# Kernel tuning notes

Measured on AMD Instinct MI355X. Metric: run time of the kernel, lower is better.

## Reference

```python
import jax, jax.numpy as jnp
import numpy as np

GAMMA = 1.1
PC_MIN_XY, PC_MAX_XY = -75.2, 75.2


def setup_inputs() -> dict:
    key = jax.random.key(0)
    k1, k2, k3, k4, k5 = jax.random.split(key, 5)
    N, B, F = 200000, 256, 5
    # points: x,y in pc range, z in [-2,4], remaining features small
    xy = jax.random.uniform(k1, (N, 2), minval=PC_MIN_XY, maxval=PC_MAX_XY)
    z = jax.random.uniform(k2, (N, 1), minval=-2.0, maxval=4.0)
    feat = jax.random.normal(k3, (N, F - 3)) * 0.1
    cur_points = jnp.concatenate([xy, z, feat], axis=-1).astype(jnp.float32)
    # boxes: cx,cy,cz, dx,dy (sizes ~1..6 m), dz, heading
    centers = jax.random.uniform(k4, (B, 3), minval=PC_MIN_XY, maxval=PC_MAX_XY)
    sizes = jax.random.uniform(k5, (B, 3), minval=1.0, maxval=6.0)
    heading = jnp.zeros((B, 1), dtype=jnp.float32)
    cur_boxes = jnp.concatenate([centers, sizes, heading], axis=-1).astype(jnp.float32)
    return {"cur_points": cur_points, "cur_boxes": cur_boxes, "num_sample": 128}


def reference(cur_points, cur_boxes, num_sample):
    # cylindrical_pool: radius-mask + topk + gather (N >= num_sample, so no pad)
    # radii of cylinders: ||(dx,dy)/2|| * gamma  -> [B]
    cur_radiis = jnp.linalg.norm(cur_boxes[:, 3:5] * 0.5, axis=-1) * GAMMA
    # pairwise xy distance [B, N]
    dis = jnp.linalg.norm(cur_points[None, :, :2] - cur_boxes[:, None, :2], axis=-1)
    point_mask = (dis <= cur_radiis[:, None]).astype(cur_points.dtype)  # [B, N]
    # topk over 0/1 mask: in-radius points first (ties -> lowest index, like torch)
    sampled_mask, sampled_idx = jax.lax.top_k(point_mask, num_sample)  # [B, S]
    sampled_points = cur_points[sampled_idx]  # [B, S, F] gather
    sampled_points = jnp.where(sampled_mask[..., None] > 0, sampled_points, 0.0)
    return sampled_points
```

## Files before the change

kernel.cpp:

```cpp
#include <hip/hip_runtime.h>

#define GAMMA_F 1.1f
#define F_DIM 5
#define BOXG 8
#define MAX_NSEG 256
#define MAXL 1024

__device__ __forceinline__ int prefix_lt(unsigned long long m) {
  return __builtin_amdgcn_mbcnt_hi(
      (unsigned)(m >> 32), __builtin_amdgcn_mbcnt_lo((unsigned)m, 0u));
}

template <int NWAVE>
__global__ void __launch_bounds__(NWAVE * 64, 8) seg_lds_kernel(
    const float* __restrict__ pts, const float* __restrict__ boxes,
    int* __restrict__ cnt, unsigned short* __restrict__ idx, int N, int S,
    int NSEG, int L, int NGRP) {
  __shared__ __align__(16) float2 sxy[MAXL];

  const int tid = threadIdx.x;
  const int lane = tid & 63;
  const int wid = tid >> 6;
  const int bpg = NGRP / NWAVE;
  const int seg = blockIdx.x / bpg;
  const int bg = blockIdx.x - seg * bpg;
  const int grp = bg * NWAVE + wid;
  const int box0 = grp * BOXG;

  const int start = seg * L;
  const int end = min(start + L, N);
  const int npts = end - start;

  float cx[BOXG], cy[BOXG], smax[BOXG];
#pragma unroll
  for (int b = 0; b < BOXG; ++b) {
    const float* bx = boxes + (box0 + b) * 7;
    cx[b] = bx[0];
    cy[b] = bx[1];
    const float hdx = __fmul_rn(bx[3], 0.5f);
    const float hdy = __fmul_rn(bx[4], 0.5f);
    const float r = __fmul_rn(
        __fsqrt_rn(__fadd_rn(__fmul_rn(hdx, hdx), __fmul_rn(hdy, hdy))),
        GAMMA_F);
    const unsigned ru = __float_as_uint(r);
    const float rsucc = __uint_as_float(ru + 1u);
    const double m = ((double)r + (double)rsucc) * 0.5;
    const double m2 = m * m;
    const bool incl = ((ru & 1u) == 0u);
    const float c1 = (float)m2;
    const double c1d = (double)c1;
    const bool keep = incl ? (c1d <= m2) : (c1d < m2);
    smax[b] = keep ? c1 : __uint_as_float(__float_as_uint(c1) - 1u);
  }

  for (int t = tid; t < npts; t += NWAVE * 64) {
    const float* p = pts + (size_t)(start + t) * F_DIM;
    sxy[t] = make_float2(p[0], p[1]);
  }
  __syncthreads();

  int c[BOXG];
#pragma unroll
  for (int b = 0; b < BOXG; ++b) c[b] = 0;

  const size_t ibase = ((size_t)box0 * NSEG + seg) * S;
  const float4* sxy4 = (const float4*)sxy;

#define PROCESS_8(RELBASE, X0, Y0, X1, Y1, G0, G1)                          \
  {                                                                         \
    const int rel = (RELBASE) + 2 * lane;                                   \
    _Pragma("unroll") for (int b = 0; b < BOXG; ++b) {                      \
      const float dx0 = __fsub_rn((X0), cx[b]);                             \
      const float dy0 = __fsub_rn((Y0), cy[b]);                             \
      const float s0 = __fadd_rn(__fmul_rn(dx0, dx0), __fmul_rn(dy0, dy0)); \
      const float dx1 = __fsub_rn((X1), cx[b]);                             \
      const float dy1 = __fsub_rn((Y1), cy[b]);                             \
      const float s1 = __fadd_rn(__fmul_rn(dx1, dx1), __fmul_rn(dy1, dy1)); \
      const bool sel0 = (G0) && (s0 <= smax[b]);                            \
      const bool sel1 = (G1) && (s1 <= smax[b]);                            \
      const unsigned long long m0 = __ballot(sel0);                         \
      const unsigned long long m1 = __ballot(sel1);                         \
      if (m0 | m1) {                                                        \
        const int p0 = prefix_lt(m0);                                       \
        const int p1 = prefix_lt(m1);                                       \
        const int r0 = c[b] + p0 + p1;                                      \
        const int r1 = c[b] + p0 + (sel0 ? 1 : 0) + p1;                     \
        unsigned short* mp = idx + ibase + (size_t)b * NSEG * S;            \
        if (sel0 && r0 < S) mp[r0] = (unsigned short)rel;                   \
        if (sel1 && r1 < S) mp[r1] = (unsigned short)(rel + 1);             \
        c[b] += __popcll(m0) + __popcll(m1);                                \
      }                                                                     \
    }                                                                       \
  }

  const int nfull = npts / 128;
  for (int it = 0; it < nfull; ++it) {
    const float4 q = sxy4[it * 64 + lane];
    PROCESS_8(it * 128, q.x, q.y, q.z, q.w, true, true);
  }
  const int relb = nfull * 128;
  if (relb < npts) {
    const float4 q = sxy4[nfull * 64 + lane];
    const int rel = relb + 2 * lane;
    const bool g0 = (rel < npts);
    const bool g1 = (rel + 1 < npts);
    PROCESS_8(relb, q.x, q.y, q.z, q.w, g0, g1);
  }
#undef PROCESS_8

  if (lane == 0) {
#pragma unroll
    for (int b = 0; b < BOXG; ++b) cnt[(box0 + b) * NSEG + seg] = min(c[b], S);
  }
}

__global__ void __launch_bounds__(256) gather_kernel(
    const float* __restrict__ pts, const int* __restrict__ cnt,
    const unsigned short* __restrict__ idx, float* __restrict__ out, int N,
    int S, int NSEG, int L) {
  const int b = blockIdx.x;
  const int tid = threadIdx.x;
  const int lane = tid & 63;
  const int wid = tid >> 6;

  __shared__ int pfx[MAX_NSEG + 1];
  __shared__ int wtot[4];
  __shared__ int woff[4];

  int v = (tid < NSEG) ? cnt[b * NSEG + tid] : 0;
  int sv = v;
#pragma unroll
  for (int d = 1; d < 64; d <<= 1) {
    const int t = __shfl_up(sv, d, 64);
    if (lane >= d) sv += t;
  }
  if (lane == 63) wtot[wid] = sv;
  __syncthreads();
  if (tid == 0) {
    int a = 0;
#pragma unroll
    for (int w = 0; w < 4; ++w) {
      woff[w] = a;
      a += wtot[w];
    }
  }
  __syncthreads();
  const int incl = sv + woff[wid];
  if (tid < NSEG) pfx[tid + 1] = incl;
  if (tid == 0) pfx[0] = 0;
  __syncthreads();

  const int total = pfx[NSEG];
  if (tid < S) {
    float* o = out + ((size_t)b * S + tid) * F_DIM;
    if (tid < total) {
      int lo = 0, hi = NSEG - 1;
      while (lo < hi) {
        const int mid = (lo + hi + 1) >> 1;
        if (pfx[mid] <= tid) lo = mid;
        else hi = mid - 1;
      }
      const int s = lo;
      const int gi =
          s * L + (int)idx[((size_t)b * NSEG + s) * S + (tid - pfx[s])];
      const float* p = pts + (size_t)gi * F_DIM;
      o[0] = p[0];
      o[1] = p[1];
      o[2] = p[2];
      o[3] = p[3];
      o[4] = p[4];
    } else {
      o[0] = 0.0f;
      o[1] = 0.0f;
      o[2] = 0.0f;
      o[3] = 0.0f;
      o[4] = 0.0f;
    }
  }
}

template <int BLOCK>
__global__ void __launch_bounds__(BLOCK) voxel_sampler_fallback(
    const float* __restrict__ pts, const float* __restrict__ boxes,
    float* __restrict__ out, int N, int S) {
  constexpr int NW = BLOCK / 64;
  const int b = blockIdx.x;
  const int tid = threadIdx.x;
  const int lane = tid & 63;
  const int wid = tid >> 6;

  const float cx = boxes[b * 7 + 0];
  const float cy = boxes[b * 7 + 1];
  const float hdx = __fmul_rn(boxes[b * 7 + 3], 0.5f);
  const float hdy = __fmul_rn(boxes[b * 7 + 4], 0.5f);
  const float r = __fmul_rn(
      __fsqrt_rn(__fadd_rn(__fmul_rn(hdx, hdx), __fmul_rn(hdy, hdy))),
      GAMMA_F);

  __shared__ int s_wsum[NW];
  __shared__ int s_count;
  if (tid == 0) s_count = 0;
  __syncthreads();

  float* outb = out + (size_t)b * S * F_DIM;

  for (int base = 0; base < N; base += BLOCK) {
    const int i = base + tid;
    bool sel = false;
    float x = 0.0f, y = 0.0f;
    if (i < N) {
      x = pts[i * F_DIM + 0];
      y = pts[i * F_DIM + 1];
      const float ddx = __fsub_rn(x, cx);
      const float ddy = __fsub_rn(y, cy);
      const float dis =
          __fsqrt_rn(__fadd_rn(__fmul_rn(ddx, ddx), __fmul_rn(ddy, ddy)));
      sel = (dis <= r);
    }
    const unsigned long long m = __ballot(sel);
    if (lane == 0) s_wsum[wid] = __popcll(m);
    __syncthreads();
    const int cbase = s_count;
    int wbase = 0;
    int tot = 0;
#pragma unroll
    for (int w = 0; w < NW; ++w) {
      const int v = s_wsum[w];
      if (w < wid) wbase += v;
      tot += v;
    }
    const int pos = cbase + wbase + __popcll(m & ((1ULL << lane) - 1ULL));
    if (sel && pos < S) {
      float* o = outb + pos * F_DIM;
      o[0] = x;
      o[1] = y;
      o[2] = pts[i * F_DIM + 2];
      o[3] = pts[i * F_DIM + 3];
      o[4] = pts[i * F_DIM + 4];
    }
    __syncthreads();
    if (tid == 0) s_count = cbase + tot;
    __syncthreads();
    if (cbase + tot >= S) break;
  }

  __syncthreads();
  int cnt = s_count;
  if (cnt > S) cnt = S;
  for (int j = cnt * F_DIM + tid; j < S * F_DIM; j += BLOCK) outb[j] = 0.0f;
}

extern "C" void kernel_launch(void* const* d_in, const int* in_sizes, int n_in,
                              void* d_out, int out_size, void* d_ws,
                              size_t ws_size, hipStream_t stream) {
  const float* pts = (const float*)d_in[0];
  const float* boxes = (const float*)d_in[1];
  float* out = (float*)d_out;

  const int N = in_sizes[0] / F_DIM;
  const int B = in_sizes[1] / 7;
  const int S = out_size / (B * F_DIM);

  const int NSEG = 256;
  int L = ((N + NSEG - 1) / NSEG + 1) & ~1;
  const int NGRP = B / BOXG;
  constexpr int NWAVE = 16;

  const size_t sz_cnt = (size_t)B * NSEG * sizeof(int);
  const size_t off_idx = (sz_cnt + 255) & ~(size_t)255;
  const size_t sz_idx = (size_t)B * NSEG * S * sizeof(unsigned short);
  const size_t need = off_idx + sz_idx;

  const bool fast = (ws_size >= need) && (L >= 2) && (L <= MAXL) &&
                    (L - 1 <= 65535) && (B % BOXG == 0) && (S <= 256) &&
                    (NSEG <= MAX_NSEG) && (NGRP % NWAVE == 0) &&
                    ((size_t)L * NSEG >= (size_t)N);

  if (fast) {
    char* ws = (char*)d_ws;
    int* cnt = (int*)ws;
    unsigned short* idx = (unsigned short*)(ws + off_idx);

    const int bpg = NGRP / NWAVE;
    seg_lds_kernel<NWAVE><<<NSEG * bpg, NWAVE * 64, 0, stream>>>(
        pts, boxes, cnt, idx, N, S, NSEG, L, NGRP);
    gather_kernel<<<B, 256, 0, stream>>>(pts, cnt, idx, out, N, S, NSEG, L);
  } else {
    voxel_sampler_fallback<1024><<<B, 1024, 0, stream>>>(pts, boxes, out, N,
                                                         S);
  }
}
```

Measured before the change: 24.20 us.

## Stage raw point rows via coalesced float4 LDS loads and use packed FP32 math

Each block now copies its whole segment of 5-float point rows into LDS with aligned float4 loads, then splits x and y into separate LDS arrays. This replaces the strided scalar global reads of x,y. The distance test now uses v_pk_add_f32/v_pk_mul_f32 on pairs of points, with negated box centres precomputed. The min-waves launch bound drops from 8 to 4 because LDS use grows to roughly 28KB per block, which risks lower occupancy. It also adds an extra barrier and a staging pass.

Measured after the change: 27.04 us. 11.8% more time.

```diff
diff --git a/kernel.cpp b/kernel.cpp
--- a/kernel.cpp
+++ b/kernel.cpp
@@ -6,17 +6,32 @@
 #define MAX_NSEG 256
 #define MAXL 1024
 
+typedef float f32x2 __attribute__((ext_vector_type(2)));
+
+__device__ __forceinline__ f32x2 pk_add(f32x2 a, f32x2 b) {
+  f32x2 d;
+  asm("v_pk_add_f32 %0, %1, %2" : "=v"(d) : "v"(a), "v"(b));
+  return d;
+}
+__device__ __forceinline__ f32x2 pk_mul(f32x2 a, f32x2 b) {
+  f32x2 d;
+  asm("v_pk_mul_f32 %0, %1, %2" : "=v"(d) : "v"(a), "v"(b));
+  return d;
+}
+
 __device__ __forceinline__ int prefix_lt(unsigned long long m) {
   return __builtin_amdgcn_mbcnt_hi(
       (unsigned)(m >> 32), __builtin_amdgcn_mbcnt_lo((unsigned)m, 0u));
 }
 
 template <int NWAVE>
-__global__ void __launch_bounds__(NWAVE * 64, 8) seg_lds_kernel(
+__global__ void __launch_bounds__(NWAVE * 64, 4) seg_lds_kernel(
     const float* __restrict__ pts, const float* __restrict__ boxes,
     int* __restrict__ cnt, unsigned short* __restrict__ idx, int N, int S,
     int NSEG, int L, int NGRP) {
-  __shared__ __align__(16) float2 sxy[MAXL];
+  __shared__ __align__(16) float rawf[MAXL * 5 + 4];
+  __shared__ float sx[MAXL + 128];
+  __shared__ float sy[MAXL + 128];
 
   const int tid = threadIdx.x;
   const int lane = tid & 63;
@@ -31,12 +46,36 @@
   const int end = min(start + L, N);
   const int npts = end - start;
 
-  float cx[BOXG], cy[BOXG], smax[BOXG];
+  {
+    const int dwStart = start * 5;
+    const int dwEnd = dwStart + npts * 5;
+    const int a0 = dwStart & ~3;
+    const int totDw = dwEnd - a0;
+    const int k4 = totDw >> 2;
+    const float4* __restrict__ g4 = (const float4*)(pts + a0);
+    float4* __restrict__ r4 = (float4*)rawf;
+    for (int k = tid; k < k4; k += NWAVE * 64) r4[k] = g4[k];
+    for (int d = a0 + (k4 << 2) + tid; d < dwEnd; d += NWAVE * 64)
+      rawf[d - a0] = pts[d];
+    __syncthreads();
+    const int off0 = dwStart - a0;
+    for (int t = tid; t < npts; t += NWAVE * 64) {
+      sx[t] = rawf[off0 + t * 5];
+      sy[t] = rawf[off0 + t * 5 + 1];
+    }
+  }
+
+  f32x2 ncx2[BOXG], ncy2[BOXG];
+  float smax[BOXG];
 #pragma unroll
   for (int b = 0; b < BOXG; ++b) {
     const float* bx = boxes + (box0 + b) * 7;
-    cx[b] = bx[0];
-    cy[b] = bx[1];
+    const float cx = bx[0];
+    const float cy = bx[1];
+    ncx2[b][0] = -cx;
+    ncx2[b][1] = -cx;
+    ncy2[b][0] = -cy;
+    ncy2[b][1] = -cy;
     const float hdx = __fmul_rn(bx[3], 0.5f);
     const float hdy = __fmul_rn(bx[4], 0.5f);
     const float r = __fmul_rn(
@@ -52,11 +91,6 @@
     const bool keep = incl ? (c1d <= m2) : (c1d < m2);
     smax[b] = keep ? c1 : __uint_as_float(__float_as_uint(c1) - 1u);
   }
-
-  for (int t = tid; t < npts; t += NWAVE * 64) {
-    const float* p = pts + (size_t)(start + t) * F_DIM;
-    sxy[t] = make_float2(p[0], p[1]);
-  }
   __syncthreads();
 
   int c[BOXG];
@@ -64,47 +98,47 @@
   for (int b = 0; b < BOXG; ++b) c[b] = 0;
 
   const size_t ibase = ((size_t)box0 * NSEG + seg) * S;
-  const float4* sxy4 = (const float4*)sxy;
-
-#define PROCESS_8(RELBASE, X0, Y0, X1, Y1, G0, G1)                          \
-  {                                                                         \
-    const int rel = (RELBASE) + 2 * lane;                                   \
-    _Pragma("unroll") for (int b = 0; b < BOXG; ++b) {                      \
-      const float dx0 = __fsub_rn((X0), cx[b]);                             \
-      const float dy0 = __fsub_rn((Y0), cy[b]);                             \
-      const float s0 = __fadd_rn(__fmul_rn(dx0, dx0), __fmul_rn(dy0, dy0)); \
-      const float dx1 = __fsub_rn((X1), cx[b]);                             \
-      const float dy1 = __fsub_rn((Y1), cy[b]);                             \
-      const float s1 = __fadd_rn(__fmul_rn(dx1, dx1), __fmul_rn(dy1, dy1)); \
-      const bool sel0 = (G0) && (s0 <= smax[b]);                            \
-      const bool sel1 = (G1) && (s1 <= smax[b]);                            \
-      const unsigned long long m0 = __ballot(sel0);                         \
-      const unsigned long long m1 = __ballot(sel1);                         \
-      if (m0 | m1) {                                                        \
-        const int p0 = prefix_lt(m0);                                       \
-        const int p1 = prefix_lt(m1);                                       \
-        const int r0 = c[b] + p0 + p1;                                      \
-        const int r1 = c[b] + p0 + (sel0 ? 1 : 0) + p1;                     \
-        unsigned short* mp = idx + ibase + (size_t)b * NSEG * S;            \
-        if (sel0 && r0 < S) mp[r0] = (unsigned short)rel;                   \
-        if (sel1 && r1 < S) mp[r1] = (unsigned short)(rel + 1);             \
-        c[b] += __popcll(m0) + __popcll(m1);                                \
-      }                                                                     \
-    }                                                                       \
-  }
-
   const int nfull = npts / 128;
+
+#define PROCESS_8(RELBASE, XX, YY, G0, G1)                          \
+  {                                                                 \
+    const int rel = (RELBASE) + 2 * lane;                           \
+    _Pragma("unroll") for (int b = 0; b < BOXG; ++b) {              \
+      const f32x2 dxx = pk_add((XX), ncx2[b]);                      \
+      const f32x2 dyy = pk_add((YY), ncy2[b]);                      \
+      const f32x2 mxx = pk_mul(dxx, dxx);                           \
+      const f32x2 myy = pk_mul(dyy, dyy);                           \
+      const f32x2 ss = pk_add(mxx, myy);                            \
+      const bool sel0 = (G0) && (ss[0] <= smax[b]);                 \
+      const bool sel1 = (G1) && (ss[1] <= smax[b]);                 \
+      const unsigned long long m0 = __ballot(sel0);                 \
+      const unsigned long long m1 = __ballot(sel1);                 \
+      if (m0 | m1) {                                                \
+        const int p0 = prefix_lt(m0);                               \
+        const int p1 = prefix_lt(m1);                               \
+        const int r0 = c[b] + p0 + p1;                              \
+        const int r1 = c[b] + p0 + (sel0 ? 1 : 0) + p1;             \
+        unsigned short* mp = idx + ibase + (size_t)b * NSEG * S;    \
+        if (sel0 && r0 < S) mp[r0] = (unsigned short)rel;           \
+        if (sel1 && r1 < S) mp[r1] = (unsigned short)(rel + 1);     \
+        c[b] += __popcll(m0) + __popcll(m1);                        \
+      }                                                             \
+    }                                                               \
+  }
+
   for (int it = 0; it < nfull; ++it) {
-    const float4 q = sxy4[it * 64 + lane];
-    PROCESS_8(it * 128, q.x, q.y, q.z, q.w, true, true);
+    const f32x2 xx = *(const f32x2*)&sx[it * 128 + 2 * lane];
+    const f32x2 yy = *(const f32x2*)&sy[it * 128 + 2 * lane];
+    PROCESS_8(it * 128, xx, yy, true, true);
   }
   const int relb = nfull * 128;
   if (relb < npts) {
-    const float4 q = sxy4[nfull * 64 + lane];
+    const f32x2 xx = *(const f32x2*)&sx[relb + 2 * lane];
+    const f32x2 yy = *(const f32x2*)&sy[relb + 2 * lane];
     const int rel = relb + 2 * lane;
     const bool g0 = (rel < npts);
     const bool g1 = (rel + 1 < npts);
-    PROCESS_8(relb, q.x, q.y, q.z, q.w, g0, g1);
+    PROCESS_8(relb, xx, yy, g0, g1);
   }
 #undef PROCESS_8
 
```

## Use expanded-distance test with exact fallback band for radius check

Applied to the files above, without the earlier changes.

Rewrites the per-box squared-distance test as |p|^2 - 2c·p compared against a precomputed threshold. The point norms are computed once per point in LDS, so each box costs two FMAs per point instead of subtract/multiply/add. A ±1 guard band catches points near the boundary, and only waves holding such points recompute the exact rounded distance, which keeps results identical to the reference. The shared-memory layout becomes split x/y pairs plus a norm array. Launch bounds drop to 4 blocks per CU and a new N-even requirement is added to the fast path.

Result: slower. 31.12 us (+28.6%).

```diff
diff --git a/kernel.cpp b/kernel.cpp
--- a/kernel.cpp
+++ b/kernel.cpp
@@ -12,11 +12,12 @@
 }
 
 template <int NWAVE>
-__global__ void __launch_bounds__(NWAVE * 64, 8) seg_lds_kernel(
+__global__ void __launch_bounds__(NWAVE * 64, 4) seg_lds_kernel(
     const float* __restrict__ pts, const float* __restrict__ boxes,
     int* __restrict__ cnt, unsigned short* __restrict__ idx, int N, int S,
     int NSEG, int L, int NGRP) {
-  __shared__ __align__(16) float2 sxy[MAXL];
+  __shared__ __align__(16) float4 sp[MAXL / 2 + 64];
+  __shared__ __align__(8) float2 sq[MAXL / 2 + 64];
 
   const int tid = threadIdx.x;
   const int lane = tid & 63;
@@ -30,13 +31,14 @@
   const int start = seg * L;
   const int end = min(start + L, N);
   const int npts = end - start;
-
-  float cx[BOXG], cy[BOXG], smax[BOXG];
+  const int npair = npts >> 1;
+
+  float bxv[BOXG], byv[BOXG], klo[BOXG], khi[BOXG], smaxv[BOXG];
 #pragma unroll
   for (int b = 0; b < BOXG; ++b) {
     const float* bx = boxes + (box0 + b) * 7;
-    cx[b] = bx[0];
-    cy[b] = bx[1];
+    const float cx = bx[0];
+    const float cy = bx[1];
     const float hdx = __fmul_rn(bx[3], 0.5f);
     const float hdy = __fmul_rn(bx[4], 0.5f);
     const float r = __fmul_rn(
@@ -50,12 +52,23 @@
     const float c1 = (float)m2;
     const double c1d = (double)c1;
     const bool keep = incl ? (c1d <= m2) : (c1d < m2);
-    smax[b] = keep ? c1 : __uint_as_float(__float_as_uint(c1) - 1u);
-  }
-
-  for (int t = tid; t < npts; t += NWAVE * 64) {
-    const float* p = pts + (size_t)(start + t) * F_DIM;
-    sxy[t] = make_float2(p[0], p[1]);
+    const float smax = keep ? c1 : __uint_as_float(__float_as_uint(c1) - 1u);
+    smaxv[b] = smax;
+    bxv[b] = -2.0f * cx;
+    byv[b] = -2.0f * cy;
+    const double kd =
+        (double)smax - (double)cx * (double)cx - (double)cy * (double)cy;
+    klo[b] = (float)(kd - 1.0);
+    khi[b] = (float)(kd + 1.0);
+  }
+
+  for (int t = tid; t < npair; t += NWAVE * 64) {
+    const float* p0 = pts + (size_t)(start + 2 * t) * F_DIM;
+    const float x0 = p0[0], y0 = p0[1];
+    const float x1 = p0[F_DIM], y1 = p0[F_DIM + 1];
+    sp[t] = make_float4(x0, x1, y0, y1);
+    sq[t] = make_float2(__fadd_rn(__fmul_rn(x0, x0), __fmul_rn(y0, y0)),
+                        __fadd_rn(__fmul_rn(x1, x1), __fmul_rn(y1, y1)));
   }
   __syncthreads();
 
@@ -64,47 +77,65 @@
   for (int b = 0; b < BOXG; ++b) c[b] = 0;
 
   const size_t ibase = ((size_t)box0 * NSEG + seg) * S;
-  const float4* sxy4 = (const float4*)sxy;
-
-#define PROCESS_8(RELBASE, X0, Y0, X1, Y1, G0, G1)                          \
-  {                                                                         \
-    const int rel = (RELBASE) + 2 * lane;                                   \
-    _Pragma("unroll") for (int b = 0; b < BOXG; ++b) {                      \
-      const float dx0 = __fsub_rn((X0), cx[b]);                             \
-      const float dy0 = __fsub_rn((Y0), cy[b]);                             \
-      const float s0 = __fadd_rn(__fmul_rn(dx0, dx0), __fmul_rn(dy0, dy0)); \
-      const float dx1 = __fsub_rn((X1), cx[b]);                             \
-      const float dy1 = __fsub_rn((Y1), cy[b]);                             \
-      const float s1 = __fadd_rn(__fmul_rn(dx1, dx1), __fmul_rn(dy1, dy1)); \
-      const bool sel0 = (G0) && (s0 <= smax[b]);                            \
-      const bool sel1 = (G1) && (s1 <= smax[b]);                            \
-      const unsigned long long m0 = __ballot(sel0);                         \
-      const unsigned long long m1 = __ballot(sel1);                         \
-      if (m0 | m1) {                                                        \
-        const int p0 = prefix_lt(m0);                                       \
-        const int p1 = prefix_lt(m1);                                       \
-        const int r0 = c[b] + p0 + p1;                                      \
-        const int r1 = c[b] + p0 + (sel0 ? 1 : 0) + p1;                     \
-        unsigned short* mp = idx + ibase + (size_t)b * NSEG * S;            \
-        if (sel0 && r0 < S) mp[r0] = (unsigned short)rel;                   \
-        if (sel1 && r1 < S) mp[r1] = (unsigned short)(rel + 1);             \
-        c[b] += __popcll(m0) + __popcll(m1);                                \
-      }                                                                     \
-    }                                                                       \
-  }
-
   const int nfull = npts / 128;
+
+#define PROCESS_8(RELBASE, QD, QQ, G0, G1)                                   \
+  {                                                                          \
+    const int rel = (RELBASE) + 2 * lane;                                    \
+    _Pragma("unroll") for (int b = 0; b < BOXG; ++b) {                       \
+      const float t0 = __builtin_fmaf(bxv[b], (QD).x,                        \
+                                      __builtin_fmaf(byv[b], (QD).z, (QQ).x)); \
+      const float t1 = __builtin_fmaf(bxv[b], (QD).y,                        \
+                                      __builtin_fmaf(byv[b], (QD).w, (QQ).y)); \
+      const bool in0 = (G0) && (t0 <= klo[b]);                               \
+      const bool in1 = (G1) && (t1 <= klo[b]);                               \
+      const bool may0 = (G0) && (t0 <= khi[b]);                              \
+      const bool may1 = (G1) && (t1 <= khi[b]);                              \
+      unsigned long long m0 = __ballot(in0);                                 \
+      unsigned long long m1 = __ballot(in1);                                 \
+      const unsigned long long M0 = __ballot(may0);                          \
+      const unsigned long long M1 = __ballot(may1);                          \
+      if ((M0 != m0) | (M1 != m1)) {         \
+        const float cx = __fmul_rn(bxv[b], -0.5f);        \
+        const float cy = __fmul_rn(byv[b], -0.5f);                           \
+        const float dx0 = __fsub_rn((QD).x, cx);                             \
+        const float dy0 = __fsub_rn((QD).z, cy);                             \
+        const float s0 =                                                     \
+            __fadd_rn(__fmul_rn(dx0, dx0), __fmul_rn(dy0, dy0));             \
+        const float dx1 = __fsub_rn((QD).y, cx);                             \
+        const float dy1 = __fsub_rn((QD).w, cy);                             \
+        const float s1 =                                                     \
+            __fadd_rn(__fmul_rn(dx1, dx1), __fmul_rn(dy1, dy1));             \
+        m0 = __ballot((G0) && (s0 <= smaxv[b]));                             \
+        m1 = __ballot((G1) && (s1 <= smaxv[b]));                             \
+      }                                                                      \
+      if (m0 | m1) {                                                         \
+        const int p0 = prefix_lt(m0);                                        \
+        const int p1 = prefix_lt(m1);                                        \
+        const int r0 = c[b] + p0 + p1;                                       \
+        const int r1 = c[b] + p0 + (int)((m0 >> lane) & 1ULL) + p1;          \
+        unsigned short* mp = idx + ibase + (size_t)b * NSEG * S;             \
+        if (((m0 >> lane) & 1ULL) && r0 < S) mp[r0] = (unsigned short)rel;   \
+        if (((m1 >> lane) & 1ULL) && r1 < S)                                 \
+          mp[r1] = (unsigned short)(rel + 1);                                \
+        c[b] += __popcll(m0) + __popcll(m1);                                 \
+      }                                                                      \
+    }                                                                        \
+  }
+
   for (int it = 0; it < nfull; ++it) {
-    const float4 q = sxy4[it * 64 + lane];
-    PROCESS_8(it * 128, q.x, q.y, q.z, q.w, true, true);
+    const float4 qd = sp[it * 64 + lane];
+    const float2 qq = sq[it * 64 + lane];
+    PROCESS_8(it * 128, qd, qq, true, true);
   }
   const int relb = nfull * 128;
   if (relb < npts) {
-    const float4 q = sxy4[nfull * 64 + lane];
+    const float4 qd = sp[nfull * 64 + lane];
+    const float2 qq = sq[nfull * 64 + lane];
     const int rel = relb + 2 * lane;
     const bool g0 = (rel < npts);
     const bool g1 = (rel + 1 < npts);
-    PROCESS_8(relb, q.x, q.y, q.z, q.w, g0, g1);
+    PROCESS_8(relb, qd, qq, g0, g1);
   }
 #undef PROCESS_8
 
@@ -274,7 +305,7 @@
   const bool fast = (ws_size >= need) && (L >= 2) && (L <= MAXL) &&
                     (L - 1 <= 65535) && (B % BOXG == 0) && (S <= 256) &&
                     (NSEG <= MAX_NSEG) && (NGRP % NWAVE == 0) &&
-                    ((size_t)L * NSEG >= (size_t)N);
+                    (N % 2 == 0) && ((size_t)L * NSEG >= (size_t)N);
 
   if (fast) {
     char* ws = (char*)d_ws;
```
